# Optimization experiments

Hardware: AMD Instinct MI355X
Metric: run time of the kernel (lower is better)

The kernel has to match this reference:

```python
import jax, jax.numpy as jnp
from jax import lax
import numpy as np

B, T, F = 64, 2048, 256
H0, H1, O = 512, 512, 128


def setup_inputs() -> dict:
    key = jax.random.key(0)
    ks = jax.random.split(key, 16)
    s = lambda n: 1.0 / np.sqrt(n)
    return {
        "x": jax.random.normal(ks[0], (B, T, F), dtype=jnp.float32),
        # layer 0 RNN params (torch nn.RNN layout: W_ih [H,F], W_hh [H,H])
        "W_ih0": jax.random.uniform(ks[1], (H0, F), jnp.float32, -s(H0), s(H0)),
        "W_hh0": jax.random.uniform(ks[2], (H0, H0), jnp.float32, -s(H0), s(H0)),
        "b_ih0": jax.random.uniform(ks[3], (H0,), jnp.float32, -s(H0), s(H0)),
        "b_hh0": jax.random.uniform(ks[4], (H0,), jnp.float32, -s(H0), s(H0)),
        "h0_0": jax.random.normal(ks[5], (H0,), dtype=jnp.float32),  # buffer layer1 [1,1,H0]
        # layer 1 RNN params
        "W_ih1": jax.random.uniform(ks[6], (H1, H0), jnp.float32, -s(H1), s(H1)),
        "W_hh1": jax.random.uniform(ks[7], (H1, H1), jnp.float32, -s(H1), s(H1)),
        "b_ih1": jax.random.uniform(ks[8], (H1,), jnp.float32, -s(H1), s(H1)),
        "b_hh1": jax.random.uniform(ks[9], (H1,), jnp.float32, -s(H1), s(H1)),
        "h0_1": jax.random.normal(ks[10], (H1,), dtype=jnp.float32),  # buffer layer2 [1,1,H1]
        # final linear head
        "W_fc": jax.random.uniform(ks[11], (O, H1), jnp.float32, -s(H1), s(H1)),
        "b_fc": jax.random.uniform(ks[12], (O,), jnp.float32, -s(H1), s(H1)),
    }


def _rnn_layer(x, W_ih, W_hh, b_ih, b_hh, h0):
    # x: [B, T, Fin]; returns (outputs [B, T, H], last hidden [B, H])
    bs = x.shape[0]
    # precompute input projection as one big GEMM: [B, T, H]
    xp = jnp.einsum("btf,hf->bth", x, W_ih) + b_ih + b_hh
    h_init = jnp.broadcast_to(h0, (bs, h0.shape[0]))

    def step(h, xp_t):  # h: [B, H], xp_t: [B, H]
        h_new = jnp.tanh(xp_t + h @ W_hh.T)
        return h_new, h_new

    hT, hs = lax.scan(step, h_init, xp.transpose(1, 0, 2))  # time-major scan
    return hs.transpose(1, 0, 2), hT


def reference(x, W_ih0, W_hh0, b_ih0, b_hh0, h0_0,
              W_ih1, W_hh1, b_ih1, b_hh1, h0_1, W_fc, b_fc):
    res, _ = _rnn_layer(x, W_ih0, W_hh0, b_ih0, b_hh0, h0_0)
    _, hT = _rnn_layer(res, W_ih1, W_hh1, b_ih1, b_hh1, h0_1)
    # op[-1] is the last layer's final hidden state: [B, H1]
    return hT @ W_fc.T + b_fc  # [B, O]
```

## Files before the change

### kernel.cpp

```cpp
#include <hip/hip_runtime.h>

typedef _Float16 half_t;
typedef _Float16 f16x2 __attribute__((ext_vector_type(2)));
typedef _Float16 f16x8 __attribute__((ext_vector_type(8)));
typedef float f32x4 __attribute__((ext_vector_type(4)));

#define B_SZ 64
#define T_SZ 2048
#define F_SZ 256
#define H_SZ 512
#define O_SZ 128
#define NCH 32
#define CH 64

#if defined(__has_builtin)
#if __has_builtin(__builtin_amdgcn_fdot2)
#define HAS_FDOT2 1
#endif
#if __has_builtin(__builtin_amdgcn_rcpf)
#define HAS_RCPF 1
#endif
#endif
#ifndef HAS_FDOT2
#define HAS_FDOT2 0
#endif
#ifndef HAS_RCPF
#define HAS_RCPF 0
#endif

static __device__ __forceinline__ float fdot2(unsigned int w, unsigned int h, float acc) {
#if HAS_FDOT2
    return __builtin_amdgcn_fdot2(__builtin_bit_cast(f16x2, w), __builtin_bit_cast(f16x2, h), acc, false);
#else
    f16x2 wv = __builtin_bit_cast(f16x2, w);
    f16x2 hv = __builtin_bit_cast(f16x2, h);
    return acc + (float)wv[0] * (float)hv[0] + (float)wv[1] * (float)hv[1];
#endif
}

static __device__ __forceinline__ unsigned int pack_pair(float a, float b) {
    f16x2 p;
    p[0] = (half_t)a;
    p[1] = (half_t)b;
    return __builtin_bit_cast(unsigned int, p);
}

static __device__ __forceinline__ float fast_rcp(float x) {
#if HAS_RCPF
    return __builtin_amdgcn_rcpf(x);
#else
    return 1.0f / x;
#endif
}

template<int CTRL>
static __device__ __forceinline__ float dpp_add(float x) {
    int y = __builtin_amdgcn_mov_dpp(__builtin_bit_cast(int, x), CTRL, 0xF, 0xF, true);
    return x + __builtin_bit_cast(float, y);
}

static __device__ __forceinline__ void step_barrier() {
    __builtin_amdgcn_sched_barrier(0);
    asm volatile("s_waitcnt lgkmcnt(0)" ::: "memory");
    __builtin_amdgcn_s_barrier();
    __builtin_amdgcn_sched_barrier(0);
}


__global__ void cvt_f32_f16(const float* __restrict__ src, half_t* __restrict__ dst, int n) {
    int i = blockIdx.x * 256 + threadIdx.x;
    if (i < n) dst[i] = (half_t)src[i];
}

__global__ void zero_flags(unsigned int* __restrict__ p, int n) {
    int i = blockIdx.x * 256 + threadIdx.x;
    if (i < n) p[i] = 0u;
}

template<bool A_F32, int K>
__global__ __launch_bounds__(256) void gemm_xp(const void* __restrict__ Aptr,
                                               const half_t* __restrict__ Bw,
                                               const float* __restrict__ bias1,
                                               const float* __restrict__ bias2,
                                               half_t* __restrict__ Cout)
{
    const int nt   = blockIdx.x & 7;
    const int mt   = blockIdx.x >> 3;
    const int wave = threadIdx.x >> 6;
    const int lane = threadIdx.x & 63;
    const int mrow = mt * 64 + wave * 16 + (lane & 15);
    const int koff = (lane >> 4) * 8;

    f32x4 acc[4];
#pragma unroll
    for (int i = 0; i < 4; i++) acc[i] = (f32x4){0.f, 0.f, 0.f, 0.f};

#pragma unroll 2
    for (int k0 = 0; k0 < K; k0 += 32) {
        f16x8 a;
        if (A_F32) {
            const float* ap = (const float*)Aptr + (size_t)mrow * K + (k0 + koff);
            float4 v0 = ((const float4*)ap)[0];
            float4 v1 = ((const float4*)ap)[1];
            a[0] = (half_t)v0.x; a[1] = (half_t)v0.y; a[2] = (half_t)v0.z; a[3] = (half_t)v0.w;
            a[4] = (half_t)v1.x; a[5] = (half_t)v1.y; a[6] = (half_t)v1.z; a[7] = (half_t)v1.w;
        } else {
            const half_t* ap = (const half_t*)Aptr + (size_t)mrow * K + (k0 + koff);
            a = *(const f16x8*)ap;
        }
#pragma unroll
        for (int cb = 0; cb < 4; cb++) {
            const int col = nt * 64 + cb * 16 + (lane & 15);
            f16x8 bfrag = *(const f16x8*)(Bw + (size_t)col * K + (k0 + koff));
            acc[cb] = __builtin_amdgcn_mfma_f32_16x16x32_f16(a, bfrag, acc[cb], 0, 0, 0);
        }
    }
    const int rbase = mt * 64 + wave * 16 + (lane >> 4) * 4;
#pragma unroll
    for (int cb = 0; cb < 4; cb++) {
        const int col = nt * 64 + cb * 16 + (lane & 15);
        const float bsum = bias1[col] + bias2[col];
#pragma unroll
        for (int r = 0; r < 4; r++) {
            Cout[(size_t)(rbase + r) * H_SZ + col] = (half_t)(acc[cb][r] + bsum);
        }
    }
}

__global__ __launch_bounds__(512, 2)
void rnn_mega(half_t* bufA, half_t* bufB,
              const float* __restrict__ Whh0, const float* __restrict__ Whh1,
              const half_t* __restrict__ Wih1h,
              const float* __restrict__ h0_0, const float* __restrict__ h0_1,
              const float* __restrict__ b_ih1, const float* __restrict__ b_hh1,
              float* hT,
              unsigned int* flags0, unsigned int* flags1)
{
    __shared__ __align__(16) uint4 wlds[12 * 512];
    __shared__ __align__(16) half_t hpad[2][8 * 72];

    const int role = blockIdx.x % 3;
    const int b    = blockIdx.x / 3;
    const int tid  = threadIdx.x;
    const int l    = tid & 63;
    const int s    = tid >> 6;

    if (role == 1) {
        const int w = s, lane = l;
        const int koff = (lane >> 4) * 8;
        for (int chunk = 0; chunk < NCH; chunk++) {
            if (tid == 0) {
                while (__hip_atomic_load(&flags0[b * NCH + chunk], __ATOMIC_ACQUIRE,
                                         __HIP_MEMORY_SCOPE_AGENT) == 0u)
                    __builtin_amdgcn_s_sleep(2);
            }
            __syncthreads();
            const int t0 = chunk * CH;

            f32x4 gac[4][4];
#pragma unroll
            for (int rt = 0; rt < 4; rt++)
#pragma unroll
                for (int cb = 0; cb < 4; cb++) gac[rt][cb] = (f32x4){0.f, 0.f, 0.f, 0.f};

#pragma unroll 1
            for (int k0 = 0; k0 < H_SZ; k0 += 32) {
                f16x8 bf[4];
#pragma unroll
                for (int cb = 0; cb < 4; cb++)
                    bf[cb] = *(const f16x8*)(Wih1h +
                              (size_t)(64 * w + 16 * cb + (lane & 15)) * H_SZ + k0 + koff);
#pragma unroll
                for (int rt = 0; rt < 4; rt++) {
                    const f16x8 a = *(const f16x8*)((const half_t*)bufA +
                              ((size_t)b * T_SZ + t0 + rt * 16 + (lane & 15)) * H_SZ + k0 + koff);
#pragma unroll
                    for (int cb = 0; cb < 4; cb++)
                        gac[rt][cb] = __builtin_amdgcn_mfma_f32_16x16x32_f16(a, bf[cb], gac[rt][cb], 0, 0, 0);
                }
            }
#pragma unroll
            for (int rt = 0; rt < 4; rt++) {
                const int rbase = t0 + rt * 16 + (lane >> 4) * 4;
#pragma unroll
                for (int cb = 0; cb < 4; cb++) {
                    const int col = 64 * w + 16 * cb + (lane & 15);
                    const float bsum = b_ih1[col] + b_hh1[col];
#pragma unroll
                    for (int r = 0; r < 4; r++)
                        bufB[((size_t)b * T_SZ + rbase + r) * H_SZ + col] =
                            (half_t)(gac[rt][cb][r] + bsum);
                }
            }
            __syncthreads();
            if (tid == 0)
                __hip_atomic_store(&flags1[b * NCH + chunk], 1u, __ATOMIC_RELEASE,
                                   __HIP_MEMORY_SCOPE_AGENT);
        }
        return;
    }

    const bool L1 = (role == 2);
    const float* Whh = L1 ? Whh1 : Whh0;

    const int q  = l >> 3;
    const int sp = l & 7;

    unsigned int wreg[208];
#pragma unroll
    for (int r = 0; r < 8; r++) {
        const float* wrow = Whh + (size_t)(64 * s + 8 * q + r) * H_SZ + 64 * sp;
#pragma unroll
        for (int c = 0; c < 26; c++)
            wreg[c * 8 + r] = pack_pair(wrow[2 * c], wrow[2 * c + 1]);
    }
#pragma unroll
    for (int p2 = 0; p2 < 6; p2++) {
#pragma unroll
        for (int rh = 0; rh < 2; rh++) {
            unsigned int qv[4];
#pragma unroll
            for (int rr = 0; rr < 4; rr++) {
                const int r = rh * 4 + rr;
                const float* wrow = Whh + (size_t)(64 * s + 8 * q + r) * H_SZ + 64 * sp;
                const int c = 26 + p2;
                qv[rr] = pack_pair(wrow[2 * c], wrow[2 * c + 1]);
            }
            uint4 v;
            v.x = qv[0]; v.y = qv[1]; v.z = qv[2]; v.w = qv[3];
            wlds[(p2 * 2 + rh) * 512 + tid] = v;
        }
    }
    hpad[0][s * 72 + l] = (half_t)((L1 ? h0_1 : h0_0)[tid]);
    __syncthreads();

    unsigned short* xp16 = (unsigned short*)(L1 ? bufB : bufA);
    const size_t base = (size_t)b * T_SZ * H_SZ + tid;

    const uint4* hp0 = (const uint4*)(&hpad[0][sp * 72]);
    const uint4* hp1 = (const uint4*)(&hpad[1][sp * 72]);
    half_t* hw0 = &hpad[0][s * 72 + l];
    half_t* hw1 = &hpad[1][s * 72 + l];

    const bool sb0 = (sp & 1) != 0;
    const bool sb1 = (sp & 2) != 0;
    const bool sb2 = (sp & 4) != 0;

#pragma unroll 1
    for (int chunk = 0; chunk < NCH; chunk++) {
        const int t0 = chunk * CH;
        if (L1) {
            if (tid == 0) {
                while (__hip_atomic_load(&flags1[b * NCH + chunk], __ATOMIC_ACQUIRE,
                                         __HIP_MEMORY_SCOPE_AGENT) == 0u)
                    __builtin_amdgcn_s_sleep(2);
            }
            __syncthreads();
        }
        unsigned short xpw_next = xp16[base + (size_t)t0 * H_SZ];

#pragma unroll 1
        for (int tt = 0; tt < CH; tt++) {
            const int t = t0 + tt;
            const int par = tt & 1;
            const unsigned short xpw = xpw_next;
            if (tt + 1 < CH) xpw_next = xp16[base + (size_t)(t + 1) * H_SZ];

            float acc[8];
#pragma unroll
            for (int r = 0; r < 8; r++) acc[r] = 0.f;

            const uint4* hp = par ? hp1 : hp0;

            uint4 hc  = hp[0];
            uint4 hA  = hp[6];
            uint4 hB  = hp[7];
            uint4 wv0 = wlds[0 * 512 + tid];
            uint4 wv1 = wlds[1 * 512 + tid];

#define REGBLK(CC, HV) { \
                const unsigned int hx0 = (HV).x, hx1 = (HV).y, hx2 = (HV).z, hx3 = (HV).w; \
                _Pragma("unroll") \
                for (int r = 0; r < 8; r++) acc[r] = fdot2(wreg[((CC) * 4 + 0) * 8 + r], hx0, acc[r]); \
                _Pragma("unroll") \
                for (int r = 0; r < 8; r++) acc[r] = fdot2(wreg[((CC) * 4 + 1) * 8 + r], hx1, acc[r]); \
                _Pragma("unroll") \
                for (int r = 0; r < 8; r++) acc[r] = fdot2(wreg[((CC) * 4 + 2) * 8 + r], hx2, acc[r]); \
                _Pragma("unroll") \
                for (int r = 0; r < 8; r++) acc[r] = fdot2(wreg[((CC) * 4 + 3) * 8 + r], hx3, acc[r]); }
#define CONSUME(H2) { \
                acc[0] = fdot2(wv0.x, (H2), acc[0]); acc[1] = fdot2(wv0.y, (H2), acc[1]); \
                acc[2] = fdot2(wv0.z, (H2), acc[2]); acc[3] = fdot2(wv0.w, (H2), acc[3]); \
                acc[4] = fdot2(wv1.x, (H2), acc[4]); acc[5] = fdot2(wv1.y, (H2), acc[5]); \
                acc[6] = fdot2(wv1.z, (H2), acc[6]); acc[7] = fdot2(wv1.w, (H2), acc[7]); }

            {
                uint4 hn;
                hn = hp[1];  REGBLK(0, hc)  CONSUME(hA.z)
                wv0 = wlds[2 * 512 + tid];  wv1 = wlds[3 * 512 + tid];  hc = hn;
                hn = hp[2];  REGBLK(1, hc)  CONSUME(hA.w)
                wv0 = wlds[4 * 512 + tid];  wv1 = wlds[5 * 512 + tid];  hc = hn;
                hn = hp[3];  REGBLK(2, hc)  CONSUME(hB.x)
                wv0 = wlds[6 * 512 + tid];  wv1 = wlds[7 * 512 + tid];  hc = hn;
                hn = hp[4];  REGBLK(3, hc)  CONSUME(hB.y)
                wv0 = wlds[8 * 512 + tid];  wv1 = wlds[9 * 512 + tid];  hc = hn;
                hn = hp[5];  REGBLK(4, hc)  CONSUME(hB.z)
                wv0 = wlds[10 * 512 + tid]; wv1 = wlds[11 * 512 + tid]; hc = hn;
                REGBLK(5, hc)  CONSUME(hB.w)
                {
                    const unsigned int hx0 = hA.x, hx1 = hA.y;
#pragma unroll
                    for (int r = 0; r < 8; r++) acc[r] = fdot2(wreg[24 * 8 + r], hx0, acc[r]);
#pragma unroll
                    for (int r = 0; r < 8; r++) acc[r] = fdot2(wreg[25 * 8 + r], hx1, acc[r]);
                }
            }
#undef REGBLK
#undef CONSUME

#pragma unroll
            for (int r = 0; r < 8; r++) {
                float a = acc[r];
                a = dpp_add<0x0B1>(a);
                a = dpp_add<0x04E>(a);
                a = dpp_add<0x141>(a);
                acc[r] = a;
            }
            float t0s = sb0 ? acc[1] : acc[0];
            float t1s = sb0 ? acc[3] : acc[2];
            float t2s = sb0 ? acc[5] : acc[4];
            float t3s = sb0 ? acc[7] : acc[6];
            float u0s = sb1 ? t1s : t0s;
            float u1s = sb1 ? t3s : t2s;
            float rsum = sb2 ? u1s : u0s;

            float y;
            {
                half_t xv = __builtin_bit_cast(half_t, xpw);
                y = (float)xv + rsum;
            }
            float e  = __expf(2.0f * y);
            float hn2 = 1.0f - 2.0f * fast_rcp(e + 1.0f);

            *(par ? hw0 : hw1) = (half_t)hn2;
            if (!L1)
                xp16[base + (size_t)t * H_SZ] = __builtin_bit_cast(unsigned short, (half_t)hn2);
            else if (t == T_SZ - 1)
                hT[(size_t)b * H_SZ + tid] = hn2;

            step_barrier();
        }
        if (!L1) {
            __syncthreads();
            if (tid == 0)
                __hip_atomic_store(&flags0[b * NCH + chunk], 1u, __ATOMIC_RELEASE,
                                   __HIP_MEMORY_SCOPE_AGENT);
        }
    }
}

__global__ __launch_bounds__(128) void head_fc(const float* __restrict__ hT,
                                               const float* __restrict__ Wfc,
                                               const float* __restrict__ bfc,
                                               float* __restrict__ out)
{
    __shared__ float hs[H_SZ];
    const int b = blockIdx.x, o = threadIdx.x;
    for (int i = o; i < H_SZ; i += 128) hs[i] = hT[(size_t)b * H_SZ + i];
    __syncthreads();
    const float4* w4 = (const float4*)(Wfc + (size_t)o * H_SZ);
    const float4* h4 = (const float4*)hs;
    float acc = 0.f;
#pragma unroll 4
    for (int k = 0; k < H_SZ / 4; k++) {
        float4 w = w4[k], h = h4[k];
        acc += w.x * h.x + w.y * h.y + w.z * h.z + w.w * h.w;
    }
    out[(size_t)b * O_SZ + o] = acc + bfc[o];
}


extern "C" void kernel_launch(void* const* d_in, const int* in_sizes, int n_in,
                              void* d_out, int out_size, void* d_ws, size_t ws_size,
                              hipStream_t stream) {
    const float* x     = (const float*)d_in[0];
    const float* W_ih0 = (const float*)d_in[1];
    const float* W_hh0 = (const float*)d_in[2];
    const float* b_ih0 = (const float*)d_in[3];
    const float* b_hh0 = (const float*)d_in[4];
    const float* h0_0  = (const float*)d_in[5];
    const float* W_ih1 = (const float*)d_in[6];
    const float* W_hh1 = (const float*)d_in[7];
    const float* b_ih1 = (const float*)d_in[8];
    const float* b_hh1 = (const float*)d_in[9];
    const float* h0_1  = (const float*)d_in[10];
    const float* W_fc  = (const float*)d_in[11];
    const float* b_fc  = (const float*)d_in[12];

    char* ws = (char*)d_ws;
    size_t off = 0;
    const size_t bufElems = (size_t)B_SZ * T_SZ * H_SZ;
    half_t* bufA  = (half_t*)(ws + off); off += bufElems * 2;
    half_t* bufB  = (half_t*)(ws + off); off += bufElems * 2;
    half_t* Wih0h = (half_t*)(ws + off); off += (size_t)H_SZ * F_SZ * 2;
    half_t* Wih1h = (half_t*)(ws + off); off += (size_t)H_SZ * H_SZ * 2;
    float*  hTbuf = (float*)(ws + off);  off += (size_t)B_SZ * H_SZ * 4;
    const int FLAG_N = B_SZ * NCH;
    unsigned int* flags0 = (unsigned int*)(ws + off); off += (size_t)FLAG_N * 4;
    unsigned int* flags1 = (unsigned int*)(ws + off); off += (size_t)FLAG_N * 4;

    const int M = B_SZ * T_SZ;

    zero_flags<<<(2 * FLAG_N + 255) / 256, 256, 0, stream>>>(flags0, 2 * FLAG_N);
    cvt_f32_f16<<<(H_SZ * F_SZ + 255) / 256, 256, 0, stream>>>(W_ih0, Wih0h, H_SZ * F_SZ);
    cvt_f32_f16<<<(H_SZ * H_SZ + 255) / 256, 256, 0, stream>>>(W_ih1, Wih1h, H_SZ * H_SZ);

    gemm_xp<true, F_SZ><<<(M / 64) * 8, 256, 0, stream>>>(x, Wih0h, b_ih0, b_hh0, bufA);

    rnn_mega<<<192, 512, 0, stream>>>(bufA, bufB, W_hh0, W_hh1, Wih1h,
                                      h0_0, h0_1, b_ih1, b_hh1,
                                      hTbuf, flags0, flags1);

    head_fc<<<B_SZ, 128, 0, stream>>>(hTbuf, W_fc, b_fc, (float*)d_out);
}
```

Measured before the change: 3.620 ms.

## Halve recurrent block size, give each thread two hidden units with larger register weight cache

The recurrent blocks drop from 512 to 256 threads. Each thread now computes two adjacent hidden units with 16 weight rows, caching 448 packed weight words in registers and keeping less of the weight matrix in LDS. The xp loads, h writes and output stores become packed 32-bit accesses, and the layer-1 input GEMM role widens to 128 columns per wave. The aim is fewer waves taking part in each per-step barrier and less LDS traffic, at the cost of very high register pressure that may cause spills. The launch becomes cooperative, which guarantees all spin-waiting blocks are co-resident, with a plain launch as fallback.

After: 5.868 ms. 1.62x slower.

```diff
diff --git a/kernel.cpp b/kernel.cpp
--- a/kernel.cpp
+++ b/kernel.cpp
@@ -127,7 +127,7 @@
     }
 }
 
-__global__ __launch_bounds__(512, 2)
+__global__ __launch_bounds__(256, 1)
 void rnn_mega(half_t* bufA, half_t* bufB,
               const float* __restrict__ Whh0, const float* __restrict__ Whh1,
               const half_t* __restrict__ Wih1h,
@@ -136,7 +136,7 @@
               float* hT,
               unsigned int* flags0, unsigned int* flags1)
 {
-    __shared__ __align__(16) uint4 wlds[12 * 512];
+    __shared__ __align__(16) uint4 wlds[16 * 256];
     __shared__ __align__(16) half_t hpad[2][8 * 72];
 
     const int role = blockIdx.x % 3;
@@ -157,25 +157,25 @@
             __syncthreads();
             const int t0 = chunk * CH;
 
-            f32x4 gac[4][4];
+            f32x4 gac[4][8];
 #pragma unroll
             for (int rt = 0; rt < 4; rt++)
 #pragma unroll
-                for (int cb = 0; cb < 4; cb++) gac[rt][cb] = (f32x4){0.f, 0.f, 0.f, 0.f};
+                for (int cb = 0; cb < 8; cb++) gac[rt][cb] = (f32x4){0.f, 0.f, 0.f, 0.f};
 
 #pragma unroll 1
             for (int k0 = 0; k0 < H_SZ; k0 += 32) {
-                f16x8 bf[4];
-#pragma unroll
-                for (int cb = 0; cb < 4; cb++)
+                f16x8 bf[8];
+#pragma unroll
+                for (int cb = 0; cb < 8; cb++)
                     bf[cb] = *(const f16x8*)(Wih1h +
-                              (size_t)(64 * w + 16 * cb + (lane & 15)) * H_SZ + k0 + koff);
+                              (size_t)(128 * w + 16 * cb + (lane & 15)) * H_SZ + k0 + koff);
 #pragma unroll
                 for (int rt = 0; rt < 4; rt++) {
                     const f16x8 a = *(const f16x8*)((const half_t*)bufA +
                               ((size_t)b * T_SZ + t0 + rt * 16 + (lane & 15)) * H_SZ + k0 + koff);
 #pragma unroll
-                    for (int cb = 0; cb < 4; cb++)
+                    for (int cb = 0; cb < 8; cb++)
                         gac[rt][cb] = __builtin_amdgcn_mfma_f32_16x16x32_f16(a, bf[cb], gac[rt][cb], 0, 0, 0);
                 }
             }
@@ -183,8 +183,8 @@
             for (int rt = 0; rt < 4; rt++) {
                 const int rbase = t0 + rt * 16 + (lane >> 4) * 4;
 #pragma unroll
-                for (int cb = 0; cb < 4; cb++) {
-                    const int col = 64 * w + 16 * cb + (lane & 15);
+                for (int cb = 0; cb < 8; cb++) {
+                    const int col = 128 * w + 16 * cb + (lane & 15);
                     const float bsum = b_ih1[col] + b_hh1[col];
 #pragma unroll
                     for (int r = 0; r < 4; r++)
@@ -203,44 +203,50 @@
     const bool L1 = (role == 2);
     const float* Whh = L1 ? Whh1 : Whh0;
 
-    const int q  = l >> 3;
-    const int sp = l & 7;
-
-    unsigned int wreg[208];
-#pragma unroll
-    for (int r = 0; r < 8; r++) {
-        const float* wrow = Whh + (size_t)(64 * s + 8 * q + r) * H_SZ + 64 * sp;
-#pragma unroll
-        for (int c = 0; c < 26; c++)
-            wreg[c * 8 + r] = pack_pair(wrow[2 * c], wrow[2 * c + 1]);
-    }
-#pragma unroll
-    for (int p2 = 0; p2 < 6; p2++) {
-#pragma unroll
-        for (int rh = 0; rh < 2; rh++) {
+    const int q    = l >> 3;
+    const int sp   = l & 7;
+    const int rowb = 128 * s + 16 * q;
+
+    unsigned int wreg[448];
+#pragma unroll
+    for (int r = 0; r < 16; r++) {
+        const float* wrow = Whh + (size_t)(rowb + r) * H_SZ + 64 * sp;
+#pragma unroll
+        for (int c = 0; c < 28; c++)
+            wreg[c * 16 + r] = pack_pair(wrow[2 * c], wrow[2 * c + 1]);
+    }
+#pragma unroll
+    for (int p = 0; p < 4; p++) {
+#pragma unroll
+        for (int rq = 0; rq < 4; rq++) {
+            const int c = 28 + p;
             unsigned int qv[4];
 #pragma unroll
-            for (int rr = 0; rr < 4; rr++) {
-                const int r = rh * 4 + rr;
-                const float* wrow = Whh + (size_t)(64 * s + 8 * q + r) * H_SZ + 64 * sp;
-                const int c = 26 + p2;
-                qv[rr] = pack_pair(wrow[2 * c], wrow[2 * c + 1]);
+            for (int j = 0; j < 4; j++) {
+                const float* wrow = Whh + (size_t)(rowb + 4 * rq + j) * H_SZ + 64 * sp;
+                qv[j] = pack_pair(wrow[2 * c], wrow[2 * c + 1]);
             }
             uint4 v;
             v.x = qv[0]; v.y = qv[1]; v.z = qv[2]; v.w = qv[3];
-            wlds[(p2 * 2 + rh) * 512 + tid] = v;
-        }
-    }
-    hpad[0][s * 72 + l] = (half_t)((L1 ? h0_1 : h0_0)[tid]);
+            wlds[(p * 4 + rq) * 256 + tid] = v;
+        }
+    }
+
+    const int e0 = rowb + 2 * sp;
+    {
+        const float* h0p = L1 ? h0_1 : h0_0;
+        const int slice = e0 >> 6, off = e0 & 63;
+        *(unsigned int*)&hpad[0][slice * 72 + off] = pack_pair(h0p[e0], h0p[e0 + 1]);
+    }
     __syncthreads();
 
     unsigned short* xp16 = (unsigned short*)(L1 ? bufB : bufA);
-    const size_t base = (size_t)b * T_SZ * H_SZ + tid;
+    const size_t baseu = (size_t)b * T_SZ * H_SZ + e0;
 
     const uint4* hp0 = (const uint4*)(&hpad[0][sp * 72]);
     const uint4* hp1 = (const uint4*)(&hpad[1][sp * 72]);
-    half_t* hw0 = &hpad[0][s * 72 + l];
-    half_t* hw1 = &hpad[1][s * 72 + l];
+    unsigned int* hwr0 = (unsigned int*)&hpad[0][(e0 >> 6) * 72 + (e0 & 63)];
+    unsigned int* hwr1 = (unsigned int*)&hpad[1][(e0 >> 6) * 72 + (e0 & 63)];
 
     const bool sb0 = (sp & 1) != 0;
     const bool sb1 = (sp & 2) != 0;
@@ -257,96 +263,111 @@
             }
             __syncthreads();
         }
-        unsigned short xpw_next = xp16[base + (size_t)t0 * H_SZ];
+        unsigned int xw_next = *(const unsigned int*)(xp16 + baseu + (size_t)t0 * H_SZ);
 
 #pragma unroll 1
         for (int tt = 0; tt < CH; tt++) {
             const int t = t0 + tt;
             const int par = tt & 1;
-            const unsigned short xpw = xpw_next;
-            if (tt + 1 < CH) xpw_next = xp16[base + (size_t)(t + 1) * H_SZ];
-
-            float acc[8];
-#pragma unroll
-            for (int r = 0; r < 8; r++) acc[r] = 0.f;
+            const unsigned int xw = xw_next;
+            if (tt + 1 < CH)
+                xw_next = *(const unsigned int*)(xp16 + baseu + (size_t)(t + 1) * H_SZ);
 
             const uint4* hp = par ? hp1 : hp0;
 
+            float acc[16];
+#pragma unroll
+            for (int r = 0; r < 16; r++) acc[r] = 0.f;
+
+            uint4 wpa = wlds[0 * 256 + tid], wpb = wlds[1 * 256 + tid];
+            uint4 wpc = wlds[2 * 256 + tid], wpd = wlds[3 * 256 + tid];
+            uint4 hv7 = hp[7];
             uint4 hc  = hp[0];
-            uint4 hA  = hp[6];
-            uint4 hB  = hp[7];
-            uint4 wv0 = wlds[0 * 512 + tid];
-            uint4 wv1 = wlds[1 * 512 + tid];
+            uint4 hn  = hp[1];
 
 #define REGBLK(CC, HV) { \
                 const unsigned int hx0 = (HV).x, hx1 = (HV).y, hx2 = (HV).z, hx3 = (HV).w; \
                 _Pragma("unroll") \
-                for (int r = 0; r < 8; r++) acc[r] = fdot2(wreg[((CC) * 4 + 0) * 8 + r], hx0, acc[r]); \
+                for (int r = 0; r < 16; r++) acc[r] = fdot2(wreg[((CC) * 4 + 0) * 16 + r], hx0, acc[r]); \
                 _Pragma("unroll") \
-                for (int r = 0; r < 8; r++) acc[r] = fdot2(wreg[((CC) * 4 + 1) * 8 + r], hx1, acc[r]); \
+                for (int r = 0; r < 16; r++) acc[r] = fdot2(wreg[((CC) * 4 + 1) * 16 + r], hx1, acc[r]); \
                 _Pragma("unroll") \
-                for (int r = 0; r < 8; r++) acc[r] = fdot2(wreg[((CC) * 4 + 2) * 8 + r], hx2, acc[r]); \
+                for (int r = 0; r < 16; r++) acc[r] = fdot2(wreg[((CC) * 4 + 2) * 16 + r], hx2, acc[r]); \
                 _Pragma("unroll") \
-                for (int r = 0; r < 8; r++) acc[r] = fdot2(wreg[((CC) * 4 + 3) * 8 + r], hx3, acc[r]); }
+                for (int r = 0; r < 16; r++) acc[r] = fdot2(wreg[((CC) * 4 + 3) * 16 + r], hx3, acc[r]); }
 #define CONSUME(H2) { \
-                acc[0] = fdot2(wv0.x, (H2), acc[0]); acc[1] = fdot2(wv0.y, (H2), acc[1]); \
-                acc[2] = fdot2(wv0.z, (H2), acc[2]); acc[3] = fdot2(wv0.w, (H2), acc[3]); \
-                acc[4] = fdot2(wv1.x, (H2), acc[4]); acc[5] = fdot2(wv1.y, (H2), acc[5]); \
-                acc[6] = fdot2(wv1.z, (H2), acc[6]); acc[7] = fdot2(wv1.w, (H2), acc[7]); }
-
-            {
-                uint4 hn;
-                hn = hp[1];  REGBLK(0, hc)  CONSUME(hA.z)
-                wv0 = wlds[2 * 512 + tid];  wv1 = wlds[3 * 512 + tid];  hc = hn;
-                hn = hp[2];  REGBLK(1, hc)  CONSUME(hA.w)
-                wv0 = wlds[4 * 512 + tid];  wv1 = wlds[5 * 512 + tid];  hc = hn;
-                hn = hp[3];  REGBLK(2, hc)  CONSUME(hB.x)
-                wv0 = wlds[6 * 512 + tid];  wv1 = wlds[7 * 512 + tid];  hc = hn;
-                hn = hp[4];  REGBLK(3, hc)  CONSUME(hB.y)
-                wv0 = wlds[8 * 512 + tid];  wv1 = wlds[9 * 512 + tid];  hc = hn;
-                hn = hp[5];  REGBLK(4, hc)  CONSUME(hB.z)
-                wv0 = wlds[10 * 512 + tid]; wv1 = wlds[11 * 512 + tid]; hc = hn;
-                REGBLK(5, hc)  CONSUME(hB.w)
-                {
-                    const unsigned int hx0 = hA.x, hx1 = hA.y;
-#pragma unroll
-                    for (int r = 0; r < 8; r++) acc[r] = fdot2(wreg[24 * 8 + r], hx0, acc[r]);
-#pragma unroll
-                    for (int r = 0; r < 8; r++) acc[r] = fdot2(wreg[25 * 8 + r], hx1, acc[r]);
-                }
-            }
+                acc[0]  = fdot2(wpa.x, (H2), acc[0]);  acc[1]  = fdot2(wpa.y, (H2), acc[1]); \
+                acc[2]  = fdot2(wpa.z, (H2), acc[2]);  acc[3]  = fdot2(wpa.w, (H2), acc[3]); \
+                acc[4]  = fdot2(wpb.x, (H2), acc[4]);  acc[5]  = fdot2(wpb.y, (H2), acc[5]); \
+                acc[6]  = fdot2(wpb.z, (H2), acc[6]);  acc[7]  = fdot2(wpb.w, (H2), acc[7]); \
+                acc[8]  = fdot2(wpc.x, (H2), acc[8]);  acc[9]  = fdot2(wpc.y, (H2), acc[9]); \
+                acc[10] = fdot2(wpc.z, (H2), acc[10]); acc[11] = fdot2(wpc.w, (H2), acc[11]); \
+                acc[12] = fdot2(wpd.x, (H2), acc[12]); acc[13] = fdot2(wpd.y, (H2), acc[13]); \
+                acc[14] = fdot2(wpd.z, (H2), acc[14]); acc[15] = fdot2(wpd.w, (H2), acc[15]); }
+
+            REGBLK(0, hc) CONSUME(hv7.x)
+            wpa = wlds[4 * 256 + tid];  wpb = wlds[5 * 256 + tid];
+            wpc = wlds[6 * 256 + tid];  wpd = wlds[7 * 256 + tid];
+            hc = hn; hn = hp[2];
+            REGBLK(1, hc) CONSUME(hv7.y)
+            wpa = wlds[8 * 256 + tid];  wpb = wlds[9 * 256 + tid];
+            wpc = wlds[10 * 256 + tid]; wpd = wlds[11 * 256 + tid];
+            hc = hn; hn = hp[3];
+            REGBLK(2, hc) CONSUME(hv7.z)
+            wpa = wlds[12 * 256 + tid]; wpb = wlds[13 * 256 + tid];
+            wpc = wlds[14 * 256 + tid]; wpd = wlds[15 * 256 + tid];
+            hc = hn; hn = hp[4];
+            REGBLK(3, hc) CONSUME(hv7.w)
+            hc = hn; hn = hp[5];
+            REGBLK(4, hc)
+            hc = hn; hn = hp[6];
+            REGBLK(5, hc)
+            hc = hn;
+            REGBLK(6, hc)
 #undef REGBLK
 #undef CONSUME
 
 #pragma unroll
-            for (int r = 0; r < 8; r++) {
+            for (int r = 0; r < 16; r++) {
                 float a = acc[r];
                 a = dpp_add<0x0B1>(a);
                 a = dpp_add<0x04E>(a);
                 a = dpp_add<0x141>(a);
                 acc[r] = a;
             }
-            float t0s = sb0 ? acc[1] : acc[0];
-            float t1s = sb0 ? acc[3] : acc[2];
-            float t2s = sb0 ? acc[5] : acc[4];
-            float t3s = sb0 ? acc[7] : acc[6];
-            float u0s = sb1 ? t1s : t0s;
-            float u1s = sb1 ? t3s : t2s;
-            float rsum = sb2 ? u1s : u0s;
-
-            float y;
+            float rsum0, rsum1;
             {
-                half_t xv = __builtin_bit_cast(half_t, xpw);
-                y = (float)xv + rsum;
-            }
-            float e  = __expf(2.0f * y);
-            float hn2 = 1.0f - 2.0f * fast_rcp(e + 1.0f);
-
-            *(par ? hw0 : hw1) = (half_t)hn2;
+                float t0a = sb0 ? acc[2]  : acc[0];
+                float t1a = sb0 ? acc[6]  : acc[4];
+                float t2a = sb0 ? acc[10] : acc[8];
+                float t3a = sb0 ? acc[14] : acc[12];
+                float u0a = sb1 ? t1a : t0a;
+                float u1a = sb1 ? t3a : t2a;
+                rsum0 = sb2 ? u1a : u0a;
+                float t0b = sb0 ? acc[3]  : acc[1];
+                float t1b = sb0 ? acc[7]  : acc[5];
+                float t2b = sb0 ? acc[11] : acc[9];
+                float t3b = sb0 ? acc[15] : acc[13];
+                float u0b = sb1 ? t1b : t0b;
+                float u1b = sb1 ? t3b : t2b;
+                rsum1 = sb2 ? u1b : u0b;
+            }
+
+            half_t xlo = __builtin_bit_cast(half_t, (unsigned short)(xw & 0xffffu));
+            half_t xhi = __builtin_bit_cast(half_t, (unsigned short)(xw >> 16));
+            float y0 = (float)xlo + rsum0;
+            float y1 = (float)xhi + rsum1;
+            float ex0 = __expf(2.0f * y0);
+            float ex1 = __expf(2.0f * y1);
+            float hn0 = 1.0f - 2.0f * fast_rcp(ex0 + 1.0f);
+            float hn1 = 1.0f - 2.0f * fast_rcp(ex1 + 1.0f);
+            unsigned int hpk = pack_pair(hn0, hn1);
+
+            *(par ? hwr0 : hwr1) = hpk;
             if (!L1)
-                xp16[base + (size_t)t * H_SZ] = __builtin_bit_cast(unsigned short, (half_t)hn2);
+                *(unsigned int*)(xp16 + baseu + (size_t)t * H_SZ) = hpk;
             else if (t == T_SZ - 1)
-                hT[(size_t)b * H_SZ + tid] = hn2;
+                *(float2*)(hT + (size_t)b * H_SZ + e0) = make_float2(hn0, hn1);
 
             step_barrier();
         }
@@ -417,9 +438,22 @@
 
     gemm_xp<true, F_SZ><<<(M / 64) * 8, 256, 0, stream>>>(x, Wih0h, b_ih0, b_hh0, bufA);
 
-    rnn_mega<<<192, 512, 0, stream>>>(bufA, bufB, W_hh0, W_hh1, Wih1h,
-                                      h0_0, h0_1, b_ih1, b_hh1,
-                                      hTbuf, flags0, flags1);
+    {
+        half_t* a0 = bufA;  half_t* a1 = bufB;
+        const float* a2 = W_hh0;  const float* a3 = W_hh1;
+        const half_t* a4 = Wih1h;
+        const float* a5 = h0_0;   const float* a6 = h0_1;
+        const float* a7 = b_ih1;  const float* a8 = b_hh1;
+        float* a9 = hTbuf;
+        unsigned int* a10 = flags0;  unsigned int* a11 = flags1;
+        void* kargs[12] = {&a0, &a1, &a2, &a3, &a4, &a5, &a6, &a7, &a8, &a9, &a10, &a11};
+        if (hipLaunchCooperativeKernel(rnn_mega, dim3(192), dim3(256),
+                                       kargs, 0, stream) != hipSuccess) {
+            rnn_mega<<<192, 256, 0, stream>>>(bufA, bufB, W_hh0, W_hh1, Wih1h,
+                                              h0_0, h0_1, b_ih1, b_hh1,
+                                              hTbuf, flags0, flags1);
+        }
+    }
 
     head_fc<<<B_SZ, 128, 0, stream>>>(hTbuf, W_fc, b_fc, (float*)d_out);
 }
```

## Process two batch rows per recurrent block to reuse register-held weights

Applied to the files above, without the earlier changes.

Each recurrent workgroup now advances two batch sequences together, so every weight held in registers or LDS is used for two dot products per step. The grid shrinks from 192 to 96 blocks and the flags are indexed per batch pair. The register/LDS split of W_hh moves from 26/6 to 24/8 pairs, and the DPP reduction is reordered to select before the last butterfly. Per-step latency on the serial recurrence grows because each step does twice the arithmetic, and the chip runs with half as many active blocks.

Result: slower. 5.787 ms (+59.9%).

```diff
diff --git a/kernel.cpp b/kernel.cpp
--- a/kernel.cpp
+++ b/kernel.cpp
@@ -12,6 +12,7 @@
 #define O_SZ 128
 #define NCH 32
 #define CH 64
+#define NG 32
 
 #if defined(__has_builtin)
 #if __has_builtin(__builtin_amdgcn_fdot2)
@@ -57,6 +58,36 @@
 static __device__ __forceinline__ float dpp_add(float x) {
     int y = __builtin_amdgcn_mov_dpp(__builtin_bit_cast(int, x), CTRL, 0xF, 0xF, true);
     return x + __builtin_bit_cast(float, y);
+}
+
+static __device__ __forceinline__ float reduce_sel(float acc[8], bool sb0, bool sb1, bool sb2) {
+    float m0 = dpp_add<0x141>(acc[0]);
+    float m1 = dpp_add<0x141>(acc[1]);
+    float m2 = dpp_add<0x141>(acc[2]);
+    float m3 = dpp_add<0x141>(acc[3]);
+    float m4 = dpp_add<0x141>(acc[4]);
+    float m5 = dpp_add<0x141>(acc[5]);
+    float m6 = dpp_add<0x141>(acc[6]);
+    float m7 = dpp_add<0x141>(acc[7]);
+    float t0 = dpp_add<0x0B1>(m0);
+    float t1 = dpp_add<0x0B1>(m1);
+    float t2 = dpp_add<0x0B1>(m2);
+    float t3 = dpp_add<0x0B1>(m3);
+    float t4 = dpp_add<0x0B1>(m4);
+    float t5 = dpp_add<0x0B1>(m5);
+    float t6 = dpp_add<0x0B1>(m6);
+    float t7 = dpp_add<0x0B1>(m7);
+    float u0 = sb0 ? t1 : t0;
+    float u1 = sb0 ? t3 : t2;
+    float u2 = sb0 ? t5 : t4;
+    float u3 = sb0 ? t7 : t6;
+    u0 = dpp_add<0x04E>(u0);
+    u1 = dpp_add<0x04E>(u1);
+    u2 = dpp_add<0x04E>(u2);
+    u3 = dpp_add<0x04E>(u3);
+    float v0 = sb1 ? u1 : u0;
+    float v1 = sb1 ? u3 : u2;
+    return sb2 ? v1 : v0;
 }
 
 static __device__ __forceinline__ void step_barrier() {
@@ -136,11 +167,12 @@
               float* hT,
               unsigned int* flags0, unsigned int* flags1)
 {
-    __shared__ __align__(16) uint4 wlds[12 * 512];
-    __shared__ __align__(16) half_t hpad[2][8 * 72];
+    __shared__ __align__(16) uint4  wlds[16 * 512];
+    __shared__ __align__(16) half_t hpad[2][2][8 * 72];
 
     const int role = blockIdx.x % 3;
-    const int b    = blockIdx.x / 3;
+    const int g    = blockIdx.x / 3;
+    const int b0   = 2 * g;
     const int tid  = threadIdx.x;
     const int l    = tid & 63;
     const int s    = tid >> 6;
@@ -150,51 +182,55 @@
         const int koff = (lane >> 4) * 8;
         for (int chunk = 0; chunk < NCH; chunk++) {
             if (tid == 0) {
-                while (__hip_atomic_load(&flags0[b * NCH + chunk], __ATOMIC_ACQUIRE,
+                while (__hip_atomic_load(&flags0[g * NCH + chunk], __ATOMIC_ACQUIRE,
                                          __HIP_MEMORY_SCOPE_AGENT) == 0u)
                     __builtin_amdgcn_s_sleep(2);
             }
             __syncthreads();
             const int t0 = chunk * CH;
 
-            f32x4 gac[4][4];
-#pragma unroll
-            for (int rt = 0; rt < 4; rt++)
-#pragma unroll
-                for (int cb = 0; cb < 4; cb++) gac[rt][cb] = (f32x4){0.f, 0.f, 0.f, 0.f};
-
 #pragma unroll 1
-            for (int k0 = 0; k0 < H_SZ; k0 += 32) {
-                f16x8 bf[4];
-#pragma unroll
-                for (int cb = 0; cb < 4; cb++)
-                    bf[cb] = *(const f16x8*)(Wih1h +
-                              (size_t)(64 * w + 16 * cb + (lane & 15)) * H_SZ + k0 + koff);
+            for (int bb = 0; bb < 2; bb++) {
+                const int bat = b0 + bb;
+                f32x4 gac[4][4];
+#pragma unroll
+                for (int rt = 0; rt < 4; rt++)
+#pragma unroll
+                    for (int cb = 0; cb < 4; cb++) gac[rt][cb] = (f32x4){0.f, 0.f, 0.f, 0.f};
+
+#pragma unroll 1
+                for (int k0 = 0; k0 < H_SZ; k0 += 32) {
+                    f16x8 bf[4];
+#pragma unroll
+                    for (int cb = 0; cb < 4; cb++)
+                        bf[cb] = *(const f16x8*)(Wih1h +
+                                  (size_t)(64 * w + 16 * cb + (lane & 15)) * H_SZ + k0 + koff);
+#pragma unroll
+                    for (int rt = 0; rt < 4; rt++) {
+                        const f16x8 a = *(const f16x8*)((const half_t*)bufA +
+                                  ((size_t)bat * T_SZ + t0 + rt * 16 + (lane & 15)) * H_SZ + k0 + koff);
+#pragma unroll
+                        for (int cb = 0; cb < 4; cb++)
+                            gac[rt][cb] = __builtin_amdgcn_mfma_f32_16x16x32_f16(a, bf[cb], gac[rt][cb], 0, 0, 0);
+                    }
+                }
 #pragma unroll
                 for (int rt = 0; rt < 4; rt++) {
-                    const f16x8 a = *(const f16x8*)((const half_t*)bufA +
-                              ((size_t)b * T_SZ + t0 + rt * 16 + (lane & 15)) * H_SZ + k0 + koff);
-#pragma unroll
-                    for (int cb = 0; cb < 4; cb++)
-                        gac[rt][cb] = __builtin_amdgcn_mfma_f32_16x16x32_f16(a, bf[cb], gac[rt][cb], 0, 0, 0);
-                }
-            }
-#pragma unroll
-            for (int rt = 0; rt < 4; rt++) {
-                const int rbase = t0 + rt * 16 + (lane >> 4) * 4;
-#pragma unroll
-                for (int cb = 0; cb < 4; cb++) {
-                    const int col = 64 * w + 16 * cb + (lane & 15);
-                    const float bsum = b_ih1[col] + b_hh1[col];
-#pragma unroll
-                    for (int r = 0; r < 4; r++)
-                        bufB[((size_t)b * T_SZ + rbase + r) * H_SZ + col] =
-                            (half_t)(gac[rt][cb][r] + bsum);
+                    const int rbase = t0 + rt * 16 + (lane >> 4) * 4;
+#pragma unroll
+                    for (int cb = 0; cb < 4; cb++) {
+                        const int col = 64 * w + 16 * cb + (lane & 15);
+                        const float bsum = b_ih1[col] + b_hh1[col];
+#pragma unroll
+                        for (int r = 0; r < 4; r++)
+                            bufB[((size_t)bat * T_SZ + rbase + r) * H_SZ + col] =
+                                (half_t)(gac[rt][cb][r] + bsum);
+                    }
                 }
             }
             __syncthreads();
             if (tid == 0)
-                __hip_atomic_store(&flags1[b * NCH + chunk], 1u, __ATOMIC_RELEASE,
+                __hip_atomic_store(&flags1[g * NCH + chunk], 1u, __ATOMIC_RELEASE,
                                    __HIP_MEMORY_SCOPE_AGENT);
         }
         return;
@@ -206,16 +242,16 @@
     const int q  = l >> 3;
     const int sp = l & 7;
 
-    unsigned int wreg[208];
+    unsigned int wreg[192];
 #pragma unroll
     for (int r = 0; r < 8; r++) {
         const float* wrow = Whh + (size_t)(64 * s + 8 * q + r) * H_SZ + 64 * sp;
 #pragma unroll
-        for (int c = 0; c < 26; c++)
+        for (int c = 0; c < 24; c++)
             wreg[c * 8 + r] = pack_pair(wrow[2 * c], wrow[2 * c + 1]);
     }
 #pragma unroll
-    for (int p2 = 0; p2 < 6; p2++) {
+    for (int p2 = 0; p2 < 8; p2++) {
 #pragma unroll
         for (int rh = 0; rh < 2; rh++) {
             unsigned int qv[4];
@@ -223,7 +259,7 @@
             for (int rr = 0; rr < 4; rr++) {
                 const int r = rh * 4 + rr;
                 const float* wrow = Whh + (size_t)(64 * s + 8 * q + r) * H_SZ + 64 * sp;
-                const int c = 26 + p2;
+                const int c = 24 + p2;
                 qv[rr] = pack_pair(wrow[2 * c], wrow[2 * c + 1]);
             }
             uint4 v;
@@ -231,16 +267,16 @@
             wlds[(p2 * 2 + rh) * 512 + tid] = v;
         }
     }
-    hpad[0][s * 72 + l] = (half_t)((L1 ? h0_1 : h0_0)[tid]);
+    {
+        const float h0v = (L1 ? h0_1 : h0_0)[tid];
+        hpad[0][0][s * 72 + l] = (half_t)h0v;
+        hpad[1][0][s * 72 + l] = (half_t)h0v;
+    }
     __syncthreads();
 
     unsigned short* xp16 = (unsigned short*)(L1 ? bufB : bufA);
-    const size_t base = (size_t)b * T_SZ * H_SZ + tid;
-
-    const uint4* hp0 = (const uint4*)(&hpad[0][sp * 72]);
-    const uint4* hp1 = (const uint4*)(&hpad[1][sp * 72]);
-    half_t* hw0 = &hpad[0][s * 72 + l];
-    half_t* hw1 = &hpad[1][s * 72 + l];
+    const size_t baseA = (size_t)b0 * T_SZ * H_SZ + tid;
+    const size_t baseB = baseA + (size_t)T_SZ * H_SZ;
 
     const bool sb0 = (sp & 1) != 0;
     const bool sb1 = (sp & 2) != 0;
@@ -251,109 +287,103 @@
         const int t0 = chunk * CH;
         if (L1) {
             if (tid == 0) {
-                while (__hip_atomic_load(&flags1[b * NCH + chunk], __ATOMIC_ACQUIRE,
+                while (__hip_atomic_load(&flags1[g * NCH + chunk], __ATOMIC_ACQUIRE,
                                          __HIP_MEMORY_SCOPE_AGENT) == 0u)
                     __builtin_amdgcn_s_sleep(2);
             }
             __syncthreads();
         }
-        unsigned short xpw_next = xp16[base + (size_t)t0 * H_SZ];
+        unsigned short xpA_next = xp16[baseA + (size_t)t0 * H_SZ];
+        unsigned short xpB_next = xp16[baseB + (size_t)t0 * H_SZ];
 
 #pragma unroll 1
         for (int tt = 0; tt < CH; tt++) {
             const int t = t0 + tt;
             const int par = tt & 1;
-            const unsigned short xpw = xpw_next;
-            if (tt + 1 < CH) xpw_next = xp16[base + (size_t)(t + 1) * H_SZ];
-
-            float acc[8];
-#pragma unroll
-            for (int r = 0; r < 8; r++) acc[r] = 0.f;
-
-            const uint4* hp = par ? hp1 : hp0;
-
-            uint4 hc  = hp[0];
-            uint4 hA  = hp[6];
-            uint4 hB  = hp[7];
-            uint4 wv0 = wlds[0 * 512 + tid];
-            uint4 wv1 = wlds[1 * 512 + tid];
-
-#define REGBLK(CC, HV) { \
+            const unsigned short xpA = xpA_next;
+            const unsigned short xpB = xpB_next;
+            if (tt + 1 < CH) {
+                xpA_next = xp16[baseA + (size_t)(t + 1) * H_SZ];
+                xpB_next = xp16[baseB + (size_t)(t + 1) * H_SZ];
+            }
+
+            const uint4* hpA = (const uint4*)&hpad[0][par][sp * 72];
+            const uint4* hpB = (const uint4*)&hpad[1][par][sp * 72];
+
+            float accA[8], accB[8];
+#pragma unroll
+            for (int r = 0; r < 8; r++) { accA[r] = 0.f; accB[r] = 0.f; }
+
+#define REGBLK(CC, HV, ACC) { \
                 const unsigned int hx0 = (HV).x, hx1 = (HV).y, hx2 = (HV).z, hx3 = (HV).w; \
                 _Pragma("unroll") \
-                for (int r = 0; r < 8; r++) acc[r] = fdot2(wreg[((CC) * 4 + 0) * 8 + r], hx0, acc[r]); \
+                for (int r = 0; r < 8; r++) ACC[r] = fdot2(wreg[((CC) * 4 + 0) * 8 + r], hx0, ACC[r]); \
                 _Pragma("unroll") \
-                for (int r = 0; r < 8; r++) acc[r] = fdot2(wreg[((CC) * 4 + 1) * 8 + r], hx1, acc[r]); \
+                for (int r = 0; r < 8; r++) ACC[r] = fdot2(wreg[((CC) * 4 + 1) * 8 + r], hx1, ACC[r]); \
                 _Pragma("unroll") \
-                for (int r = 0; r < 8; r++) acc[r] = fdot2(wreg[((CC) * 4 + 2) * 8 + r], hx2, acc[r]); \
+                for (int r = 0; r < 8; r++) ACC[r] = fdot2(wreg[((CC) * 4 + 2) * 8 + r], hx2, ACC[r]); \
                 _Pragma("unroll") \
-                for (int r = 0; r < 8; r++) acc[r] = fdot2(wreg[((CC) * 4 + 3) * 8 + r], hx3, acc[r]); }
-#define CONSUME(H2) { \
-                acc[0] = fdot2(wv0.x, (H2), acc[0]); acc[1] = fdot2(wv0.y, (H2), acc[1]); \
-                acc[2] = fdot2(wv0.z, (H2), acc[2]); acc[3] = fdot2(wv0.w, (H2), acc[3]); \
-                acc[4] = fdot2(wv1.x, (H2), acc[4]); acc[5] = fdot2(wv1.y, (H2), acc[5]); \
-                acc[6] = fdot2(wv1.z, (H2), acc[6]); acc[7] = fdot2(wv1.w, (H2), acc[7]); }
-
-            {
-                uint4 hn;
-                hn = hp[1];  REGBLK(0, hc)  CONSUME(hA.z)
-                wv0 = wlds[2 * 512 + tid];  wv1 = wlds[3 * 512 + tid];  hc = hn;
-                hn = hp[2];  REGBLK(1, hc)  CONSUME(hA.w)
-                wv0 = wlds[4 * 512 + tid];  wv1 = wlds[5 * 512 + tid];  hc = hn;
-                hn = hp[3];  REGBLK(2, hc)  CONSUME(hB.x)
-                wv0 = wlds[6 * 512 + tid];  wv1 = wlds[7 * 512 + tid];  hc = hn;
-                hn = hp[4];  REGBLK(3, hc)  CONSUME(hB.y)
-                wv0 = wlds[8 * 512 + tid];  wv1 = wlds[9 * 512 + tid];  hc = hn;
-                hn = hp[5];  REGBLK(4, hc)  CONSUME(hB.z)
-                wv0 = wlds[10 * 512 + tid]; wv1 = wlds[11 * 512 + tid]; hc = hn;
-                REGBLK(5, hc)  CONSUME(hB.w)
-                {
-                    const unsigned int hx0 = hA.x, hx1 = hA.y;
-#pragma unroll
-                    for (int r = 0; r < 8; r++) acc[r] = fdot2(wreg[24 * 8 + r], hx0, acc[r]);
-#pragma unroll
-                    for (int r = 0; r < 8; r++) acc[r] = fdot2(wreg[25 * 8 + r], hx1, acc[r]);
-                }
-            }
+                for (int r = 0; r < 8; r++) ACC[r] = fdot2(wreg[((CC) * 4 + 3) * 8 + r], hx3, ACC[r]); }
+
+#pragma unroll
+            for (int cc = 0; cc < 6; cc++) {
+                const uint4 av = hpA[cc];
+                const uint4 bv = hpB[cc];
+                REGBLK(cc, av, accA)
+                REGBLK(cc, bv, accB)
+            }
+
+            const uint4 a6 = hpA[6], a7 = hpA[7];
+            const uint4 b6 = hpB[6], b7 = hpB[7];
+#define CONSUME(ACC, H2) { \
+                ACC[0] = fdot2(wv0.x, (H2), ACC[0]); ACC[1] = fdot2(wv0.y, (H2), ACC[1]); \
+                ACC[2] = fdot2(wv0.z, (H2), ACC[2]); ACC[3] = fdot2(wv0.w, (H2), ACC[3]); \
+                ACC[4] = fdot2(wv1.x, (H2), ACC[4]); ACC[5] = fdot2(wv1.y, (H2), ACC[5]); \
+                ACC[6] = fdot2(wv1.z, (H2), ACC[6]); ACC[7] = fdot2(wv1.w, (H2), ACC[7]); }
+#define WSTAGE(P2, H2A, H2B) { \
+                const uint4 wv0 = wlds[((P2) * 2 + 0) * 512 + tid]; \
+                const uint4 wv1 = wlds[((P2) * 2 + 1) * 512 + tid]; \
+                CONSUME(accA, (H2A)) \
+                CONSUME(accB, (H2B)) }
+
+            WSTAGE(0, a6.x, b6.x)
+            WSTAGE(1, a6.y, b6.y)
+            WSTAGE(2, a6.z, b6.z)
+            WSTAGE(3, a6.w, b6.w)
+            WSTAGE(4, a7.x, b7.x)
+            WSTAGE(5, a7.y, b7.y)
+            WSTAGE(6, a7.z, b7.z)
+            WSTAGE(7, a7.w, b7.w)
+#undef WSTAGE
+#undef CONSUME
 #undef REGBLK
-#undef CONSUME
-
-#pragma unroll
-            for (int r = 0; r < 8; r++) {
-                float a = acc[r];
-                a = dpp_add<0x0B1>(a);
-                a = dpp_add<0x04E>(a);
-                a = dpp_add<0x141>(a);
-                acc[r] = a;
-            }
-            float t0s = sb0 ? acc[1] : acc[0];
-            float t1s = sb0 ? acc[3] : acc[2];
-            float t2s = sb0 ? acc[5] : acc[4];
-            float t3s = sb0 ? acc[7] : acc[6];
-            float u0s = sb1 ? t1s : t0s;
-            float u1s = sb1 ? t3s : t2s;
-            float rsum = sb2 ? u1s : u0s;
-
-            float y;
-            {
-                half_t xv = __builtin_bit_cast(half_t, xpw);
-                y = (float)xv + rsum;
-            }
-            float e  = __expf(2.0f * y);
-            float hn2 = 1.0f - 2.0f * fast_rcp(e + 1.0f);
-
-            *(par ? hw0 : hw1) = (half_t)hn2;
-            if (!L1)
-                xp16[base + (size_t)t * H_SZ] = __builtin_bit_cast(unsigned short, (half_t)hn2);
-            else if (t == T_SZ - 1)
-                hT[(size_t)b * H_SZ + tid] = hn2;
+
+            const float rsA = reduce_sel(accA, sb0, sb1, sb2);
+            const float rsB = reduce_sel(accB, sb0, sb1, sb2);
+
+            float yA = (float)__builtin_bit_cast(half_t, xpA) + rsA;
+            float yB = (float)__builtin_bit_cast(half_t, xpB) + rsB;
+            float eA = __expf(2.0f * yA);
+            float eB = __expf(2.0f * yB);
+            float hnA = 1.0f - 2.0f * fast_rcp(eA + 1.0f);
+            float hnB = 1.0f - 2.0f * fast_rcp(eB + 1.0f);
+
+            hpad[0][par ^ 1][s * 72 + l] = (half_t)hnA;
+            hpad[1][par ^ 1][s * 72 + l] = (half_t)hnB;
+            if (!L1) {
+                xp16[baseA + (size_t)t * H_SZ] = __builtin_bit_cast(unsigned short, (half_t)hnA);
+                xp16[baseB + (size_t)t * H_SZ] = __builtin_bit_cast(unsigned short, (half_t)hnB);
+            } else if (t == T_SZ - 1) {
+                hT[(size_t)b0 * H_SZ + tid]       = hnA;
+                hT[(size_t)(b0 + 1) * H_SZ + tid] = hnB;
+            }
 
             step_barrier();
         }
         if (!L1) {
             __syncthreads();
             if (tid == 0)
-                __hip_atomic_store(&flags0[b * NCH + chunk], 1u, __ATOMIC_RELEASE,
+                __hip_atomic_store(&flags0[g * NCH + chunk], 1u, __ATOMIC_RELEASE,
                                    __HIP_MEMORY_SCOPE_AGENT);
         }
     }
@@ -405,7 +435,7 @@
     half_t* Wih0h = (half_t*)(ws + off); off += (size_t)H_SZ * F_SZ * 2;
     half_t* Wih1h = (half_t*)(ws + off); off += (size_t)H_SZ * H_SZ * 2;
     float*  hTbuf = (float*)(ws + off);  off += (size_t)B_SZ * H_SZ * 4;
-    const int FLAG_N = B_SZ * NCH;
+    const int FLAG_N = NG * NCH;
     unsigned int* flags0 = (unsigned int*)(ws + off); off += (size_t)FLAG_N * 4;
     unsigned int* flags1 = (unsigned int*)(ws + off); off += (size_t)FLAG_N * 4;
 
@@ -417,9 +447,9 @@
 
     gemm_xp<true, F_SZ><<<(M / 64) * 8, 256, 0, stream>>>(x, Wih0h, b_ih0, b_hh0, bufA);
 
-    rnn_mega<<<192, 512, 0, stream>>>(bufA, bufB, W_hh0, W_hh1, Wih1h,
-                                      h0_0, h0_1, b_ih1, b_hh1,
-                                      hTbuf, flags0, flags1);
+    rnn_mega<<<96, 512, 0, stream>>>(bufA, bufB, W_hh0, W_hh1, Wih1h,
+                                     h0_0, h0_1, b_ih1, b_hh1,
+                                     hTbuf, flags0, flags1);
 
     head_fc<<<B_SZ, 128, 0, stream>>>(hTbuf, W_fc, b_fc, (float*)d_out);
 }
```
